# Kernel tuning notes

Hardware: AMD Instinct MI355X
Metric: run time of the kernel (lower is better)

Reference implementation:

```python
import jax, jax.numpy as jnp
import numpy as np

EPS = 1e-05  # matches tf entropy epsilon


def setup_inputs() -> dict:
    key = jax.random.key(0)
    k1, k2 = jax.random.split(key)
    encodings = jax.random.normal(k1, (8192, 64), dtype=jnp.float32)
    categorical = jax.random.uniform(k2, (8192, 25), dtype=jnp.float32)
    return {"encodings": encodings, "categorical": categorical, "k": 15}


def reference(encodings, categorical, k):
    B = encodings.shape[0]
    n_components = categorical.shape[1]
    k = min(k, B // 4)  # layer clamps k to batch_size // 4

    hard_groups = jnp.argmax(categorical, axis=1)           # [B] int
    max_groups = jnp.max(categorical, axis=1)               # [B]

    # Batched brute-force kNN. tf.norm's sqrt is monotonic, so the strict
    # comparison `dist < kth_dist` is identical on squared distances; working
    # in squared space avoids sqrt(0) issues and an extra pass.
    sq = jnp.sum(encodings * encodings, axis=1)             # [B]
    d2 = sq[:, None] + sq[None, :] - 2.0 * (encodings @ encodings.T)
    d2 = jnp.maximum(d2, 0.0)                               # [B, B]

    # (k+1)-smallest distances per row (0-indexed k, self-distance included,
    # matching tf.gather(tf.sort(distances), k)).
    neg_topk, _ = jax.lax.top_k(-d2, k + 1)                 # [B, k+1]
    kth = -neg_topk[:, k]                                   # [B] k-th smallest

    mask = (d2 < kth[:, None]).astype(jnp.float32)          # [B, B] strict <

    # Per-row label histogram over the neighborhood: counts[i,c] = #neighbors
    # of i in cluster c. Zero bins contribute 0 to -sum(b*log(b+eps)), same as
    # tf.bincount's variable-length output.
    onehot = jax.nn.one_hot(hard_groups, n_components, dtype=jnp.float32)
    counts = mask @ onehot                                  # [B, n_components]
    n_i = jnp.sum(counts, axis=-1, keepdims=True)           # [B, 1]
    bins = counts / jnp.maximum(n_i, 1.0)
    neighbourhood_entropy = -jnp.sum(bins * jnp.log(bins + EPS), axis=-1)  # [B]

    # Global cluster-size entropy + number of populated clusters.
    gcounts = jnp.sum(onehot, axis=0)                       # [n_components]
    gbins = gcounts / jnp.float32(B)
    cluster_size_entropy = -jnp.sum(gbins * jnp.log(gbins + EPS))
    n_populated = jnp.sum(gcounts > 0).astype(jnp.float32)

    return encodings, neighbourhood_entropy, cluster_size_entropy, n_populated, max_groups
```

## Files before the change

kernel.cpp:

```cpp
#include <hip/hip_runtime.h>
#include <math.h>

#define Bsz    8192
#define Dd     64
#define NC     25
#define RT     16
#define TILES  64
#define KCAP   16
#define EPSf   1e-5f

typedef short  short8  __attribute__((ext_vector_type(8)));
typedef float  floatx4 __attribute__((ext_vector_type(4)));


__device__ inline unsigned short f2bf(float x) {
    unsigned u = __float_as_uint(x);
    u += 0x7FFFu + ((u >> 16) & 1u);
    return (unsigned short)(u >> 16);
}
__device__ inline float bf2f(unsigned short h) { return __uint_as_float(((unsigned)h) << 16); }

__device__ inline void bsort16(unsigned* a) {
    #pragma unroll
    for (int k = 2; k <= 16; k <<= 1)
        #pragma unroll
        for (int j = k >> 1; j > 0; j >>= 1)
            #pragma unroll
            for (int i = 0; i < 16; ++i) {
                int l = i ^ j;
                if (l > i) {
                    bool up = ((i & k) == 0) || (k == 16);
                    unsigned x = a[i], y = a[l];
                    unsigned lo = (x < y) ? x : y, hi = (x < y) ? y : x;
                    a[i] = up ? lo : hi;
                    a[l] = up ? hi : lo;
                }
            }
}
__device__ inline void bclean16(unsigned* t) {
    #pragma unroll
    for (int j = 8; j > 0; j >>= 1)
        #pragma unroll
        for (int i = 0; i < 16; ++i) {
            int l = i ^ j;
            if (l > i) {
                unsigned x = t[i], y = t[l];
                t[i] = (x < y) ? x : y;
                t[l] = (x < y) ? y : x;
            }
        }
}
__device__ inline void bmerge16(unsigned* ls, const unsigned* b) {
    unsigned t[16];
    #pragma unroll
    for (int i = 0; i < 16; ++i) { unsigned x = ls[i], y = b[15 - i]; t[i] = (x < y) ? x : y; }
    bclean16(t);
    #pragma unroll
    for (int i = 0; i < 16; ++i) ls[i] = t[i];
}
__device__ inline void bmerge16_shfl(unsigned* ls, int mask) {
    unsigned t[16];
    #pragma unroll
    for (int i = 0; i < 16; ++i) {
        unsigned pv = (unsigned)__shfl_xor((int)ls[15 - i], mask);
        unsigned x = ls[i];
        t[i] = (x < pv) ? x : pv;
    }
    bclean16(t);
    #pragma unroll
    for (int i = 0; i < 16; ++i) ls[i] = t[i];
}


__global__ __launch_bounds__(256) void pre_kernel(
    const float* __restrict__ enc, const float* __restrict__ cat,
    unsigned int* __restrict__ slab,
    char* __restrict__ enc1, char* __restrict__ enc2,
    float* __restrict__ out_max, float* __restrict__ out_enc)
{
    const int gid = blockIdx.x * 256 + threadIdx.x;
    const int p = gid >> 5, pr = gid & 31;

    float2 ev = ((const float2*)enc)[gid];
    ((float2*)out_enc)[gid] = ev;

    float s = ev.x * ev.x + ev.y * ev.y;
    #pragma unroll
    for (int m = 1; m < 32; m <<= 1) s += __shfl_xor(s, m, 32);

    {
        const int g = p >> 4, c15p = p & 15;
        const int d0 = 2 * pr, kh = d0 >> 5, q = (d0 >> 3) & 3, e0 = d0 & 7;
        const int base = g * 4096 + kh * 1024 + (q * 16 + c15p) * 16 + e0 * 2;
        unsigned short ha = f2bf(ev.x), hb = f2bf(ev.y);
        unsigned short la = f2bf(ev.x - bf2f(ha)), lb = f2bf(ev.y - bf2f(hb));
        *(unsigned*)(enc1 + base)        = (unsigned)ha | ((unsigned)hb << 16);
        *(unsigned*)(enc1 + base + 2048) = (unsigned)la | ((unsigned)lb << 16);
        float y0 = -2.f * ev.x, y1 = -2.f * ev.y;
        unsigned short hc = f2bf(y0), hd = f2bf(y1);
        unsigned short lc = f2bf(y0 - bf2f(hc)), ld = f2bf(y1 - bf2f(hd));
        *(unsigned*)(enc2 + base)        = (unsigned)hc | ((unsigned)hd << 16);
        *(unsigned*)(enc2 + base + 2048) = (unsigned)lc | ((unsigned)ld << 16);
    }
    float cv = (pr < NC) ? cat[p * NC + pr] : -1.f;
    int ci = pr;
    #pragma unroll
    for (int m = 1; m < 32; m <<= 1) {
        float ov = __shfl_xor(cv, m, 32);
        int   oi = __shfl_xor(ci, m, 32);
        if (ov > cv || (ov == cv && oi < ci)) { cv = ov; ci = oi; }
    }
    if (pr == 0) {
        out_max[p] = cv;
        slab[p] = (__float_as_uint(s) & ~31u) | (unsigned)ci;
    }
}

__global__ __launch_bounds__(512, 4) void main_kernel(
    const char* __restrict__ enc1, const char* __restrict__ enc2,
    const unsigned int* __restrict__ slab, const int* __restrict__ kptr,
    float* __restrict__ out_ent, float* __restrict__ out_glob)
{
    __shared__ unsigned wl[8 * 16 * 17];
    __shared__ int cnt[32];

    const int tid  = threadIdx.x, bid = blockIdx.x;
    const int wv   = tid >> 6, lane = tid & 63;
    const int quad = (tid >> 4) & 3, c15 = tid & 15;
    const int rowbase = bid * RT;

    short8 bh[2], bl[2];
    {
        const char* ib = enc1 + (size_t)bid * 4096 + lane * 16;
        bh[0] = *(const short8*)(ib);
        bh[1] = *(const short8*)(ib + 1024);
        bl[0] = *(const short8*)(ib + 2048);
        bl[1] = *(const short8*)(ib + 3072);
    }
    const float sqi = __uint_as_float(slab[rowbase + c15] & ~31u);

    unsigned ls[KCAP];
    #pragma unroll
    for (int q = 0; q < KCAP; ++q) ls[q] = 0xFFFFFFFFu;
    unsigned cand[16];

    const char* jp = enc2 + (size_t)wv * 4096 + lane * 16;
    const unsigned* sp = slab + wv * 16 + quad * 4;

    for (int t = 0; t < TILES; t += 2) {
        short8 ah0 = *(const short8*)(jp);
        short8 ah1 = *(const short8*)(jp + 1024);
        short8 al0 = *(const short8*)(jp + 2048);
        short8 al1 = *(const short8*)(jp + 3072);
        uint4  sva = *(const uint4*)(sp);
        short8 ch0 = *(const short8*)(jp + 32768);
        short8 ch1 = *(const short8*)(jp + 33792);
        short8 cl0 = *(const short8*)(jp + 34816);
        short8 cl1 = *(const short8*)(jp + 35840);
        uint4  svb = *(const uint4*)(sp + 128);
        jp += 65536; sp += 256;

        floatx4 accA = (floatx4){0.f, 0.f, 0.f, 0.f};
        floatx4 accB = (floatx4){0.f, 0.f, 0.f, 0.f};
        accA = __builtin_amdgcn_mfma_f32_16x16x32_bf16(ah0, bh[0], accA, 0, 0, 0);
        accB = __builtin_amdgcn_mfma_f32_16x16x32_bf16(ch0, bh[0], accB, 0, 0, 0);
        accA = __builtin_amdgcn_mfma_f32_16x16x32_bf16(ah0, bl[0], accA, 0, 0, 0);
        accB = __builtin_amdgcn_mfma_f32_16x16x32_bf16(ch0, bl[0], accB, 0, 0, 0);
        accA = __builtin_amdgcn_mfma_f32_16x16x32_bf16(al0, bh[0], accA, 0, 0, 0);
        accB = __builtin_amdgcn_mfma_f32_16x16x32_bf16(cl0, bh[0], accB, 0, 0, 0);
        accA = __builtin_amdgcn_mfma_f32_16x16x32_bf16(ah1, bh[1], accA, 0, 0, 0);
        accB = __builtin_amdgcn_mfma_f32_16x16x32_bf16(ch1, bh[1], accB, 0, 0, 0);
        accA = __builtin_amdgcn_mfma_f32_16x16x32_bf16(ah1, bl[1], accA, 0, 0, 0);
        accB = __builtin_amdgcn_mfma_f32_16x16x32_bf16(ch1, bl[1], accB, 0, 0, 0);
        accA = __builtin_amdgcn_mfma_f32_16x16x32_bf16(al1, bh[1], accA, 0, 0, 0);
        accB = __builtin_amdgcn_mfma_f32_16x16x32_bf16(cl1, bh[1], accB, 0, 0, 0);

        {
            unsigned sa[4] = {sva.x, sva.y, sva.z, sva.w};
            unsigned sb[4] = {svb.x, svb.y, svb.z, svb.w};
            #pragma unroll
            for (int r = 0; r < 4; ++r) {
                float d2a = fmaxf(sqi + __uint_as_float(sa[r] & ~31u) + accA[r], 0.f);
                cand[4 * (t & 3) + r] = (__float_as_uint(d2a) & ~31u) | (sa[r] & 31u);
                float d2b = fmaxf(sqi + __uint_as_float(sb[r] & ~31u) + accB[r], 0.f);
                cand[4 * ((t + 1) & 3) + r] = (__float_as_uint(d2b) & ~31u) | (sb[r] & 31u);
            }
        }
        if ((t & 3) == 2) {
            bsort16(cand);
            bmerge16(ls, cand);
        }
    }

    if (bid == 0) {
        if (tid < 32) cnt[tid] = 0;
        __syncthreads();
        for (int i = tid; i < Bsz; i += 512) atomicAdd(&cnt[slab[i] & 31u], 1);
        __syncthreads();
        if (tid == 0) {
            float gent = 0.f, npop = 0.f;
            for (int i = 0; i < NC; ++i) {
                int g = cnt[i];
                if (g > 0) {
                    npop += 1.f;
                    float gb = (float)g / (float)Bsz;
                    gent -= gb * logf(gb + EPSf);
                }
            }
            out_glob[0] = gent;
            out_glob[1] = npop;
        }
        __syncthreads();
    }

    bmerge16_shfl(ls, 16);
    bmerge16_shfl(ls, 32);
    if (quad == 0) {
        #pragma unroll
        for (int q = 0; q < KCAP; ++q) wl[(wv * 16 + c15) * 17 + q] = ls[q];
    }
    __syncthreads();
    if (wv == 0) {
        const int row = tid >> 2, sub = tid & 3;
        unsigned A[16], Bv[16];
        #pragma unroll
        for (int i = 0; i < 16; ++i) A[i]  = wl[((2 * sub)     * 16 + row) * 17 + i];
        #pragma unroll
        for (int i = 0; i < 16; ++i) Bv[i] = wl[((2 * sub + 1) * 16 + row) * 17 + i];
        bmerge16(A, Bv);
        bmerge16_shfl(A, 1);
        bmerge16_shfl(A, 2);

        int kk = kptr[0];
        if (kk > Bsz / 4) kk = Bsz / 4;
        if (kk > KCAP - 1) kk = KCAP - 1;

        unsigned kth = A[15];
        #pragma unroll
        for (int q = 0; q < 16; ++q) if (q == kk) kth = A[q];
        int nn = 0;
        #pragma unroll
        for (int t = 0; t < 15; ++t) nn += (t < kk && A[t] < kth) ? 1 : 0;

        float inv = 1.f / (float)((nn > 0) ? nn : 1);
        float part = 0.f;
        #pragma unroll
        for (int a4 = 0; a4 < 4; ++a4) {
            int a = sub + 4 * a4;
            if (a < nn) {
                int la = (int)(A[a] & 31u);
                int c = 0;
                #pragma unroll
                for (int b = 0; b < 15; ++b) c += (b < nn && (int)(A[b] & 31u) == la) ? 1 : 0;
                part -= inv * logf((float)c * inv + EPSf);
            }
        }
        part += __shfl_xor(part, 1);
        part += __shfl_xor(part, 2);
        if (sub == 0) out_ent[rowbase + row] = part;
    }
}

extern "C" void kernel_launch(void* const* d_in, const int* in_sizes, int n_in,
                              void* d_out, int out_size, void* d_ws, size_t ws_size,
                              hipStream_t stream)
{
    const float* enc  = (const float*)d_in[0];
    const float* cat  = (const float*)d_in[1];
    const int*   kptr = (const int*)d_in[2];
    float* out = (float*)d_out;

    unsigned int* slab = (unsigned int*)d_ws;
    char*         enc1 = (char*)d_ws + 32768;
    char*         enc2 = (char*)d_ws + 2129920;

    float* out_enc  = out;
    float* out_ent  = out + Bsz * Dd;
    float* out_glob = out + Bsz * Dd + Bsz;
    float* out_max  = out + Bsz * Dd + Bsz + 2;

    pre_kernel<<<1024, 256, 0, stream>>>(enc, cat, slab, enc1, enc2, out_max, out_enc);
    main_kernel<<<Bsz / RT, 512, 0, stream>>>(enc1, enc2, slab, kptr, out_ent, out_glob);
}
```

Baseline: 128.6 us.

## Process 32 query rows per block with 16 waves and contiguous column slices

Each block now handles two 16-row query tiles, so every column tile loaded from global memory feeds MFMAs for both row tiles, halving column-data traffic per row. Blocks grow to 1024 threads (16 waves), and each wave scans a contiguous run of 32 column tiles instead of interleaved ones. Candidates are now sorted in groups of 8 and merged into the running top-16 every iteration, and the final cross-wave merge uses 8 lanes per row. This costs more registers (two B fragments, two top-k lists) and may lower occupancy. It also changes the merge cost per candidate.

```diff
diff --git a/kernel.cpp b/kernel.cpp
--- a/kernel.cpp
+++ b/kernel.cpp
@@ -4,8 +4,7 @@
 #define Bsz    8192
 #define Dd     64
 #define NC     25
-#define RT     16
-#define TILES  64
+#define RT     32
 #define KCAP   16
 #define EPSf   1e-5f
 
@@ -20,16 +19,16 @@
 }
 __device__ inline float bf2f(unsigned short h) { return __uint_as_float(((unsigned)h) << 16); }
 
-__device__ inline void bsort16(unsigned* a) {
-    #pragma unroll
-    for (int k = 2; k <= 16; k <<= 1)
+__device__ inline void bsort8(unsigned* a) {
+    #pragma unroll
+    for (int k = 2; k <= 8; k <<= 1)
         #pragma unroll
         for (int j = k >> 1; j > 0; j >>= 1)
             #pragma unroll
-            for (int i = 0; i < 16; ++i) {
+            for (int i = 0; i < 8; ++i) {
                 int l = i ^ j;
                 if (l > i) {
-                    bool up = ((i & k) == 0) || (k == 16);
+                    bool up = ((i & k) == 0) || (k == 8);
                     unsigned x = a[i], y = a[l];
                     unsigned lo = (x < y) ? x : y, hi = (x < y) ? y : x;
                     a[i] = up ? lo : hi;
@@ -49,6 +48,16 @@
                 t[l] = (x < y) ? y : x;
             }
         }
+}
+__device__ inline void bmerge16_8(unsigned* ls, const unsigned* b) {
+    unsigned t[16];
+    #pragma unroll
+    for (int i = 0; i < 8; ++i) t[i] = ls[i];
+    #pragma unroll
+    for (int i = 8; i < 16; ++i) { unsigned x = ls[i], y = b[15 - i]; t[i] = (x < y) ? x : y; }
+    bclean16(t);
+    #pragma unroll
+    for (int i = 0; i < 16; ++i) ls[i] = t[i];
 }
 __device__ inline void bmerge16(unsigned* ls, const unsigned* b) {
     unsigned t[16];
@@ -116,12 +125,12 @@
     }
 }
 
-__global__ __launch_bounds__(512, 4) void main_kernel(
+__global__ __launch_bounds__(1024, 4) void main_kernel(
     const char* __restrict__ enc1, const char* __restrict__ enc2,
     const unsigned int* __restrict__ slab, const int* __restrict__ kptr,
     float* __restrict__ out_ent, float* __restrict__ out_glob)
 {
-    __shared__ unsigned wl[8 * 16 * 17];
+    __shared__ unsigned wl[16 * 32 * 17];
     __shared__ int cnt[32];
 
     const int tid  = threadIdx.x, bid = blockIdx.x;
@@ -129,81 +138,106 @@
     const int quad = (tid >> 4) & 3, c15 = tid & 15;
     const int rowbase = bid * RT;
 
-    short8 bh[2], bl[2];
+    short8 bh0[2], bl0[2], bh1[2], bl1[2];
     {
-        const char* ib = enc1 + (size_t)bid * 4096 + lane * 16;
-        bh[0] = *(const short8*)(ib);
-        bh[1] = *(const short8*)(ib + 1024);
-        bl[0] = *(const short8*)(ib + 2048);
-        bl[1] = *(const short8*)(ib + 3072);
-    }
-    const float sqi = __uint_as_float(slab[rowbase + c15] & ~31u);
-
-    unsigned ls[KCAP];
-    #pragma unroll
-    for (int q = 0; q < KCAP; ++q) ls[q] = 0xFFFFFFFFu;
-    unsigned cand[16];
-
-    const char* jp = enc2 + (size_t)wv * 4096 + lane * 16;
-    const unsigned* sp = slab + wv * 16 + quad * 4;
-
-    for (int t = 0; t < TILES; t += 2) {
-        short8 ah0 = *(const short8*)(jp);
-        short8 ah1 = *(const short8*)(jp + 1024);
-        short8 al0 = *(const short8*)(jp + 2048);
-        short8 al1 = *(const short8*)(jp + 3072);
-        uint4  sva = *(const uint4*)(sp);
-        short8 ch0 = *(const short8*)(jp + 32768);
-        short8 ch1 = *(const short8*)(jp + 33792);
-        short8 cl0 = *(const short8*)(jp + 34816);
-        short8 cl1 = *(const short8*)(jp + 35840);
-        uint4  svb = *(const uint4*)(sp + 128);
-        jp += 65536; sp += 256;
-
-        floatx4 accA = (floatx4){0.f, 0.f, 0.f, 0.f};
-        floatx4 accB = (floatx4){0.f, 0.f, 0.f, 0.f};
-        accA = __builtin_amdgcn_mfma_f32_16x16x32_bf16(ah0, bh[0], accA, 0, 0, 0);
-        accB = __builtin_amdgcn_mfma_f32_16x16x32_bf16(ch0, bh[0], accB, 0, 0, 0);
-        accA = __builtin_amdgcn_mfma_f32_16x16x32_bf16(ah0, bl[0], accA, 0, 0, 0);
-        accB = __builtin_amdgcn_mfma_f32_16x16x32_bf16(ch0, bl[0], accB, 0, 0, 0);
-        accA = __builtin_amdgcn_mfma_f32_16x16x32_bf16(al0, bh[0], accA, 0, 0, 0);
-        accB = __builtin_amdgcn_mfma_f32_16x16x32_bf16(cl0, bh[0], accB, 0, 0, 0);
-        accA = __builtin_amdgcn_mfma_f32_16x16x32_bf16(ah1, bh[1], accA, 0, 0, 0);
-        accB = __builtin_amdgcn_mfma_f32_16x16x32_bf16(ch1, bh[1], accB, 0, 0, 0);
-        accA = __builtin_amdgcn_mfma_f32_16x16x32_bf16(ah1, bl[1], accA, 0, 0, 0);
-        accB = __builtin_amdgcn_mfma_f32_16x16x32_bf16(ch1, bl[1], accB, 0, 0, 0);
-        accA = __builtin_amdgcn_mfma_f32_16x16x32_bf16(al1, bh[1], accA, 0, 0, 0);
-        accB = __builtin_amdgcn_mfma_f32_16x16x32_bf16(cl1, bh[1], accB, 0, 0, 0);
-
+        const char* ib = enc1 + (size_t)(bid * 2) * 4096 + lane * 16;
+        bh0[0] = *(const short8*)(ib);
+        bh0[1] = *(const short8*)(ib + 1024);
+        bl0[0] = *(const short8*)(ib + 2048);
+        bl0[1] = *(const short8*)(ib + 3072);
+        bh1[0] = *(const short8*)(ib + 4096);
+        bh1[1] = *(const short8*)(ib + 5120);
+        bl1[0] = *(const short8*)(ib + 6144);
+        bl1[1] = *(const short8*)(ib + 7168);
+    }
+    const float sqi0 = __uint_as_float(slab[rowbase + c15] & ~31u);
+    const float sqi1 = __uint_as_float(slab[rowbase + 16 + c15] & ~31u);
+
+    unsigned ls0[KCAP], ls1[KCAP];
+    #pragma unroll
+    for (int q = 0; q < KCAP; ++q) { ls0[q] = 0xFFFFFFFFu; ls1[q] = 0xFFFFFFFFu; }
+    unsigned candA[8], candB[8];
+
+    const char* jp = enc2 + (size_t)(wv * 32) * 4096 + lane * 16;
+    const unsigned* sp = slab + (wv * 32) * 16 + quad * 4;
+
+    for (int g = 0; g < 32; g += 2) {
+        short8 fh0 = *(const short8*)(jp);
+        short8 fh1 = *(const short8*)(jp + 1024);
+        short8 fl0 = *(const short8*)(jp + 2048);
+        short8 fl1 = *(const short8*)(jp + 3072);
+        short8 gh0 = *(const short8*)(jp + 4096);
+        short8 gh1 = *(const short8*)(jp + 5120);
+        short8 gl0 = *(const short8*)(jp + 6144);
+        short8 gl1 = *(const short8*)(jp + 7168);
+        uint4  sv0 = *(const uint4*)(sp);
+        uint4  sv1 = *(const uint4*)(sp + 16);
+        jp += 8192; sp += 32;
+
+        floatx4 accP = (floatx4){0.f,0.f,0.f,0.f}, accQ = (floatx4){0.f,0.f,0.f,0.f};
+        accP = __builtin_amdgcn_mfma_f32_16x16x32_bf16(fh0, bh0[0], accP, 0, 0, 0);
+        accQ = __builtin_amdgcn_mfma_f32_16x16x32_bf16(fh0, bh1[0], accQ, 0, 0, 0);
+        accP = __builtin_amdgcn_mfma_f32_16x16x32_bf16(fh0, bl0[0], accP, 0, 0, 0);
+        accQ = __builtin_amdgcn_mfma_f32_16x16x32_bf16(fh0, bl1[0], accQ, 0, 0, 0);
+        accP = __builtin_amdgcn_mfma_f32_16x16x32_bf16(fl0, bh0[0], accP, 0, 0, 0);
+        accQ = __builtin_amdgcn_mfma_f32_16x16x32_bf16(fl0, bh1[0], accQ, 0, 0, 0);
+        accP = __builtin_amdgcn_mfma_f32_16x16x32_bf16(fh1, bh0[1], accP, 0, 0, 0);
+        accQ = __builtin_amdgcn_mfma_f32_16x16x32_bf16(fh1, bh1[1], accQ, 0, 0, 0);
+        accP = __builtin_amdgcn_mfma_f32_16x16x32_bf16(fh1, bl0[1], accP, 0, 0, 0);
+        accQ = __builtin_amdgcn_mfma_f32_16x16x32_bf16(fh1, bl1[1], accQ, 0, 0, 0);
+        accP = __builtin_amdgcn_mfma_f32_16x16x32_bf16(fl1, bh0[1], accP, 0, 0, 0);
+        accQ = __builtin_amdgcn_mfma_f32_16x16x32_bf16(fl1, bh1[1], accQ, 0, 0, 0);
         {
-            unsigned sa[4] = {sva.x, sva.y, sva.z, sva.w};
-            unsigned sb[4] = {svb.x, svb.y, svb.z, svb.w};
+            unsigned sa[4] = {sv0.x, sv0.y, sv0.z, sv0.w};
             #pragma unroll
             for (int r = 0; r < 4; ++r) {
-                float d2a = fmaxf(sqi + __uint_as_float(sa[r] & ~31u) + accA[r], 0.f);
-                cand[4 * (t & 3) + r] = (__float_as_uint(d2a) & ~31u) | (sa[r] & 31u);
-                float d2b = fmaxf(sqi + __uint_as_float(sb[r] & ~31u) + accB[r], 0.f);
-                cand[4 * ((t + 1) & 3) + r] = (__float_as_uint(d2b) & ~31u) | (sb[r] & 31u);
-            }
-        }
-        if ((t & 3) == 2) {
-            bsort16(cand);
-            bmerge16(ls, cand);
-        }
+                float d2a = fmaxf(sqi0 + __uint_as_float(sa[r] & ~31u) + accP[r], 0.f);
+                candA[r] = (__float_as_uint(d2a) & ~31u) | (sa[r] & 31u);
+                float d2b = fmaxf(sqi1 + __uint_as_float(sa[r] & ~31u) + accQ[r], 0.f);
+                candB[r] = (__float_as_uint(d2b) & ~31u) | (sa[r] & 31u);
+            }
+        }
+        accP = (floatx4){0.f,0.f,0.f,0.f}; accQ = (floatx4){0.f,0.f,0.f,0.f};
+        accP = __builtin_amdgcn_mfma_f32_16x16x32_bf16(gh0, bh0[0], accP, 0, 0, 0);
+        accQ = __builtin_amdgcn_mfma_f32_16x16x32_bf16(gh0, bh1[0], accQ, 0, 0, 0);
+        accP = __builtin_amdgcn_mfma_f32_16x16x32_bf16(gh0, bl0[0], accP, 0, 0, 0);
+        accQ = __builtin_amdgcn_mfma_f32_16x16x32_bf16(gh0, bl1[0], accQ, 0, 0, 0);
+        accP = __builtin_amdgcn_mfma_f32_16x16x32_bf16(gl0, bh0[0], accP, 0, 0, 0);
+        accQ = __builtin_amdgcn_mfma_f32_16x16x32_bf16(gl0, bh1[0], accQ, 0, 0, 0);
+        accP = __builtin_amdgcn_mfma_f32_16x16x32_bf16(gh1, bh0[1], accP, 0, 0, 0);
+        accQ = __builtin_amdgcn_mfma_f32_16x16x32_bf16(gh1, bh1[1], accQ, 0, 0, 0);
+        accP = __builtin_amdgcn_mfma_f32_16x16x32_bf16(gh1, bl0[1], accP, 0, 0, 0);
+        accQ = __builtin_amdgcn_mfma_f32_16x16x32_bf16(gh1, bl1[1], accQ, 0, 0, 0);
+        accP = __builtin_amdgcn_mfma_f32_16x16x32_bf16(gl1, bh0[1], accP, 0, 0, 0);
+        accQ = __builtin_amdgcn_mfma_f32_16x16x32_bf16(gl1, bh1[1], accQ, 0, 0, 0);
+        {
+            unsigned sb[4] = {sv1.x, sv1.y, sv1.z, sv1.w};
+            #pragma unroll
+            for (int r = 0; r < 4; ++r) {
+                float d2a = fmaxf(sqi0 + __uint_as_float(sb[r] & ~31u) + accP[r], 0.f);
+                candA[4 + r] = (__float_as_uint(d2a) & ~31u) | (sb[r] & 31u);
+                float d2b = fmaxf(sqi1 + __uint_as_float(sb[r] & ~31u) + accQ[r], 0.f);
+                candB[4 + r] = (__float_as_uint(d2b) & ~31u) | (sb[r] & 31u);
+            }
+        }
+        bsort8(candA);
+        bmerge16_8(ls0, candA);
+        bsort8(candB);
+        bmerge16_8(ls1, candB);
     }
 
     if (bid == 0) {
         if (tid < 32) cnt[tid] = 0;
         __syncthreads();
-        for (int i = tid; i < Bsz; i += 512) atomicAdd(&cnt[slab[i] & 31u], 1);
+        for (int i = tid; i < Bsz; i += 1024) atomicAdd(&cnt[slab[i] & 31u], 1);
         __syncthreads();
         if (tid == 0) {
             float gent = 0.f, npop = 0.f;
             for (int i = 0; i < NC; ++i) {
-                int g = cnt[i];
-                if (g > 0) {
+                int g2 = cnt[i];
+                if (g2 > 0) {
                     npop += 1.f;
-                    float gb = (float)g / (float)Bsz;
+                    float gb = (float)g2 / (float)Bsz;
                     gent -= gb * logf(gb + EPSf);
                 }
             }
@@ -213,23 +247,27 @@
         __syncthreads();
     }
 
-    bmerge16_shfl(ls, 16);
-    bmerge16_shfl(ls, 32);
+    bmerge16_shfl(ls0, 16); bmerge16_shfl(ls0, 32);
+    bmerge16_shfl(ls1, 16); bmerge16_shfl(ls1, 32);
     if (quad == 0) {
         #pragma unroll
-        for (int q = 0; q < KCAP; ++q) wl[(wv * 16 + c15) * 17 + q] = ls[q];
+        for (int q = 0; q < KCAP; ++q) {
+            wl[(wv * 32 + c15) * 17 + q]      = ls0[q];
+            wl[(wv * 32 + 16 + c15) * 17 + q] = ls1[q];
+        }
     }
     __syncthreads();
-    if (wv == 0) {
-        const int row = tid >> 2, sub = tid & 3;
+    if (tid < 256) {
+        const int row = tid >> 3, sub = tid & 7;
         unsigned A[16], Bv[16];
         #pragma unroll
-        for (int i = 0; i < 16; ++i) A[i]  = wl[((2 * sub)     * 16 + row) * 17 + i];
-        #pragma unroll
-        for (int i = 0; i < 16; ++i) Bv[i] = wl[((2 * sub + 1) * 16 + row) * 17 + i];
+        for (int i = 0; i < 16; ++i) A[i]  = wl[((2 * sub)     * 32 + row) * 17 + i];
+        #pragma unroll
+        for (int i = 0; i < 16; ++i) Bv[i] = wl[((2 * sub + 1) * 32 + row) * 17 + i];
         bmerge16(A, Bv);
         bmerge16_shfl(A, 1);
         bmerge16_shfl(A, 2);
+        bmerge16_shfl(A, 4);
 
         int kk = kptr[0];
         if (kk > Bsz / 4) kk = Bsz / 4;
@@ -245,8 +283,8 @@
         float inv = 1.f / (float)((nn > 0) ? nn : 1);
         float part = 0.f;
         #pragma unroll
-        for (int a4 = 0; a4 < 4; ++a4) {
-            int a = sub + 4 * a4;
+        for (int a8 = 0; a8 < 2; ++a8) {
+            int a = sub + 8 * a8;
             if (a < nn) {
                 int la = (int)(A[a] & 31u);
                 int c = 0;
@@ -257,6 +295,7 @@
         }
         part += __shfl_xor(part, 1);
         part += __shfl_xor(part, 2);
+        part += __shfl_xor(part, 4);
         if (sub == 0) out_ent[rowbase + row] = part;
     }
 }
@@ -280,5 +319,5 @@
     float* out_max  = out + Bsz * Dd + Bsz + 2;
 
     pre_kernel<<<1024, 256, 0, stream>>>(enc, cat, slab, enc1, enc2, out_max, out_enc);
-    main_kernel<<<Bsz / RT, 512, 0, stream>>>(enc1, enc2, slab, kptr, out_ent, out_glob);
-}
+    main_kernel<<<Bsz / RT, 1024, 0, stream>>>(enc1, enc2, slab, kptr, out_ent, out_glob);
+}
```

Result: faster. 122.4 us (-4.8%).

## Use 16 waves per block with contiguous column chunks per wave

Applied to the files above, without the earlier changes.

Doubles the main kernel block to 1024 threads, so 16 waves each scan a contiguous chunk of 32 column tiles instead of 8 waves interleaving 64 tiles two at a time. The final cross-wave merge now spans 16 partial lists and uses 8 lanes per row with an extra shuffle-merge stage. The aim is more wave-level parallelism and shorter per-wave serial top-k loops. In exchange each wave loses the two independent MFMA accumulator chains, and register pressure under launch_bounds(1024, 8) could force spills.

```diff
diff --git a/kernel.cpp b/kernel.cpp
--- a/kernel.cpp
+++ b/kernel.cpp
@@ -5,7 +5,6 @@
 #define Dd     64
 #define NC     25
 #define RT     16
-#define TILES  64
 #define KCAP   16
 #define EPSf   1e-5f
 
@@ -116,12 +115,12 @@
     }
 }
 
-__global__ __launch_bounds__(512, 4) void main_kernel(
+__global__ __launch_bounds__(1024, 8) void main_kernel(
     const char* __restrict__ enc1, const char* __restrict__ enc2,
     const unsigned int* __restrict__ slab, const int* __restrict__ kptr,
     float* __restrict__ out_ent, float* __restrict__ out_glob)
 {
-    __shared__ unsigned wl[8 * 16 * 17];
+    __shared__ unsigned wl[16 * 16 * 17];
     __shared__ int cnt[32];
 
     const int tid  = threadIdx.x, bid = blockIdx.x;
@@ -144,49 +143,34 @@
     for (int q = 0; q < KCAP; ++q) ls[q] = 0xFFFFFFFFu;
     unsigned cand[16];
 
-    const char* jp = enc2 + (size_t)wv * 4096 + lane * 16;
-    const unsigned* sp = slab + wv * 16 + quad * 4;
-
-    for (int t = 0; t < TILES; t += 2) {
+    const char* jp = enc2 + (size_t)(wv * 32) * 4096 + lane * 16;
+    const unsigned* sp = slab + (wv * 32) * 16 + quad * 4;
+
+    for (int g = 0; g < 32; ++g) {
         short8 ah0 = *(const short8*)(jp);
         short8 ah1 = *(const short8*)(jp + 1024);
         short8 al0 = *(const short8*)(jp + 2048);
         short8 al1 = *(const short8*)(jp + 3072);
-        uint4  sva = *(const uint4*)(sp);
-        short8 ch0 = *(const short8*)(jp + 32768);
-        short8 ch1 = *(const short8*)(jp + 33792);
-        short8 cl0 = *(const short8*)(jp + 34816);
-        short8 cl1 = *(const short8*)(jp + 35840);
-        uint4  svb = *(const uint4*)(sp + 128);
-        jp += 65536; sp += 256;
-
-        floatx4 accA = (floatx4){0.f, 0.f, 0.f, 0.f};
-        floatx4 accB = (floatx4){0.f, 0.f, 0.f, 0.f};
-        accA = __builtin_amdgcn_mfma_f32_16x16x32_bf16(ah0, bh[0], accA, 0, 0, 0);
-        accB = __builtin_amdgcn_mfma_f32_16x16x32_bf16(ch0, bh[0], accB, 0, 0, 0);
-        accA = __builtin_amdgcn_mfma_f32_16x16x32_bf16(ah0, bl[0], accA, 0, 0, 0);
-        accB = __builtin_amdgcn_mfma_f32_16x16x32_bf16(ch0, bl[0], accB, 0, 0, 0);
-        accA = __builtin_amdgcn_mfma_f32_16x16x32_bf16(al0, bh[0], accA, 0, 0, 0);
-        accB = __builtin_amdgcn_mfma_f32_16x16x32_bf16(cl0, bh[0], accB, 0, 0, 0);
-        accA = __builtin_amdgcn_mfma_f32_16x16x32_bf16(ah1, bh[1], accA, 0, 0, 0);
-        accB = __builtin_amdgcn_mfma_f32_16x16x32_bf16(ch1, bh[1], accB, 0, 0, 0);
-        accA = __builtin_amdgcn_mfma_f32_16x16x32_bf16(ah1, bl[1], accA, 0, 0, 0);
-        accB = __builtin_amdgcn_mfma_f32_16x16x32_bf16(ch1, bl[1], accB, 0, 0, 0);
-        accA = __builtin_amdgcn_mfma_f32_16x16x32_bf16(al1, bh[1], accA, 0, 0, 0);
-        accB = __builtin_amdgcn_mfma_f32_16x16x32_bf16(cl1, bh[1], accB, 0, 0, 0);
+        uint4  sv  = *(const uint4*)(sp);
+        jp += 4096; sp += 16;
+
+        floatx4 acc = (floatx4){0.f, 0.f, 0.f, 0.f};
+        acc = __builtin_amdgcn_mfma_f32_16x16x32_bf16(ah0, bh[0], acc, 0, 0, 0);
+        acc = __builtin_amdgcn_mfma_f32_16x16x32_bf16(ah0, bl[0], acc, 0, 0, 0);
+        acc = __builtin_amdgcn_mfma_f32_16x16x32_bf16(al0, bh[0], acc, 0, 0, 0);
+        acc = __builtin_amdgcn_mfma_f32_16x16x32_bf16(ah1, bh[1], acc, 0, 0, 0);
+        acc = __builtin_amdgcn_mfma_f32_16x16x32_bf16(ah1, bl[1], acc, 0, 0, 0);
+        acc = __builtin_amdgcn_mfma_f32_16x16x32_bf16(al1, bh[1], acc, 0, 0, 0);
 
         {
-            unsigned sa[4] = {sva.x, sva.y, sva.z, sva.w};
-            unsigned sb[4] = {svb.x, svb.y, svb.z, svb.w};
+            unsigned sa[4] = {sv.x, sv.y, sv.z, sv.w};
             #pragma unroll
             for (int r = 0; r < 4; ++r) {
-                float d2a = fmaxf(sqi + __uint_as_float(sa[r] & ~31u) + accA[r], 0.f);
-                cand[4 * (t & 3) + r] = (__float_as_uint(d2a) & ~31u) | (sa[r] & 31u);
-                float d2b = fmaxf(sqi + __uint_as_float(sb[r] & ~31u) + accB[r], 0.f);
-                cand[4 * ((t + 1) & 3) + r] = (__float_as_uint(d2b) & ~31u) | (sb[r] & 31u);
-            }
-        }
-        if ((t & 3) == 2) {
+                float d2 = fmaxf(sqi + __uint_as_float(sa[r] & ~31u) + acc[r], 0.f);
+                cand[4 * (g & 3) + r] = (__float_as_uint(d2) & ~31u) | (sa[r] & 31u);
+            }
+        }
+        if ((g & 3) == 3) {
             bsort16(cand);
             bmerge16(ls, cand);
         }
@@ -195,15 +179,15 @@
     if (bid == 0) {
         if (tid < 32) cnt[tid] = 0;
         __syncthreads();
-        for (int i = tid; i < Bsz; i += 512) atomicAdd(&cnt[slab[i] & 31u], 1);
+        for (int i = tid; i < Bsz; i += 1024) atomicAdd(&cnt[slab[i] & 31u], 1);
         __syncthreads();
         if (tid == 0) {
             float gent = 0.f, npop = 0.f;
             for (int i = 0; i < NC; ++i) {
-                int g = cnt[i];
-                if (g > 0) {
+                int g2 = cnt[i];
+                if (g2 > 0) {
                     npop += 1.f;
-                    float gb = (float)g / (float)Bsz;
+                    float gb = (float)g2 / (float)Bsz;
                     gent -= gb * logf(gb + EPSf);
                 }
             }
@@ -220,8 +204,8 @@
         for (int q = 0; q < KCAP; ++q) wl[(wv * 16 + c15) * 17 + q] = ls[q];
     }
     __syncthreads();
-    if (wv == 0) {
-        const int row = tid >> 2, sub = tid & 3;
+    if (tid < 128) {
+        const int row = tid >> 3, sub = tid & 7;
         unsigned A[16], Bv[16];
         #pragma unroll
         for (int i = 0; i < 16; ++i) A[i]  = wl[((2 * sub)     * 16 + row) * 17 + i];
@@ -230,6 +214,7 @@
         bmerge16(A, Bv);
         bmerge16_shfl(A, 1);
         bmerge16_shfl(A, 2);
+        bmerge16_shfl(A, 4);
 
         int kk = kptr[0];
         if (kk > Bsz / 4) kk = Bsz / 4;
@@ -245,8 +230,8 @@
         float inv = 1.f / (float)((nn > 0) ? nn : 1);
         float part = 0.f;
         #pragma unroll
-        for (int a4 = 0; a4 < 4; ++a4) {
-            int a = sub + 4 * a4;
+        for (int a8 = 0; a8 < 2; ++a8) {
+            int a = sub + 8 * a8;
             if (a < nn) {
                 int la = (int)(A[a] & 31u);
                 int c = 0;
@@ -257,6 +242,7 @@
         }
         part += __shfl_xor(part, 1);
         part += __shfl_xor(part, 2);
+        part += __shfl_xor(part, 4);
         if (sub == 0) out_ent[rowbase + row] = part;
     }
 }
@@ -280,5 +266,5 @@
     float* out_max  = out + Bsz * Dd + Bsz + 2;
 
     pre_kernel<<<1024, 256, 0, stream>>>(enc, cat, slab, enc1, enc2, out_max, out_enc);
-    main_kernel<<<Bsz / RT, 512, 0, stream>>>(enc1, enc2, slab, kptr, out_ent, out_glob);
-}
+    main_kernel<<<Bsz / RT, 1024, 0, stream>>>(enc1, enc2, slab, kptr, out_ent, out_glob);
+}
```

After: 131.4 us. 1.02x slower.
